# Performance work log

Hardware: AMD Instinct MI355X
Metric: run time of the kernel (lower is better)

Reference implementation:

```python
import jax, jax.numpy as jnp
import numpy as np

EPS = 1e-4

def safe_clamp(x, max_val):
    # nan -> 0, +inf -> max_val, -inf -> -max_val, then clamp to [-max_val, max_val]
    x = jnp.where(jnp.isnan(x), 0.0, x)
    x = jnp.where(jnp.isinf(x) & (x > 0), max_val, x)
    x = jnp.where(jnp.isinf(x) & (x < 0), -max_val, x)
    return jnp.clip(x, -max_val, max_val)

def setup_inputs() -> dict:
    key = jax.random.key(0)
    k1, k2 = jax.random.split(key)
    hidden_states = jax.random.normal(k1, (4, 4096, 2048), dtype=jnp.float32)
    ln_weight = jnp.ones((2048,), dtype=jnp.float32)
    ln_bias = jnp.zeros((2048,), dtype=jnp.float32)
    gate_weight = jax.random.normal(k2, (64, 2048), dtype=jnp.float32) * 0.01
    return {"hidden_states": hidden_states, "ln_weight": ln_weight,
            "ln_bias": ln_bias, "gate_weight": gate_weight}

def reference(hidden_states, ln_weight, ln_bias, gate_weight):
    B, S, H = hidden_states.shape
    top_k = 2
    x = hidden_states.reshape(-1, H)  # (N, H)
    # LayerNorm(eps=1e-5)
    mu = jnp.mean(x, axis=-1, keepdims=True)
    var = jnp.mean((x - mu) ** 2, axis=-1, keepdims=True)
    x = (x - mu) * jax.lax.rsqrt(var + 1e-5) * ln_weight + ln_bias
    x = safe_clamp(x, 50.0)
    # gate: (N, H) @ (H, E)
    router_logits = jnp.clip(x @ gate_weight.T, -10.0, 10.0)
    # eval mode: no noise
    router_probs = jnp.clip(jax.nn.softmax(router_logits, axis=-1), EPS, 1.0)
    top_k_probs, top_k_indices = jax.lax.top_k(router_probs, top_k)
    prob_sum = jnp.maximum(jnp.sum(top_k_probs, axis=-1, keepdims=True), EPS)
    top_k_probs = top_k_probs / prob_sum
    return top_k_probs, top_k_indices, router_logits
```

## Files before the change

### kernel.cpp

```cpp
#include <hip/hip_runtime.h>
#include <math.h>

#define H 2048
#define E 64
#define MR 16
#define KCH 128
#define NCH 16
#define LR 136

typedef _Float16 half8  __attribute__((ext_vector_type(8)));
typedef _Float16 half4h __attribute__((ext_vector_type(4)));
typedef float    f32x4  __attribute__((ext_vector_type(4)));

#define MFMA16(A,B,C) __builtin_amdgcn_mfma_f32_16x16x32_f16(A,B,C,0,0,0)


__global__ __launch_bounds__(256) void prep_pack(const float* __restrict__ W,
        const float* __restrict__ lnw, _Float16* __restrict__ Bh,
        _Float16* __restrict__ Bl) {
    int idx  = blockIdx.x * 256 + threadIdx.x;
    int lane = idx & 63;
    int ks   = idx >> 8;
    int e  = ((idx >> 6) & 3) * 16 + (lane & 15);
    int k0 = ks * 32 + ((lane >> 4) << 3);
    half8 hh, ll;
    #pragma unroll
    for (int j = 0; j < 8; ++j) {
        float wf = lnw[k0 + j] * W[e * H + k0 + j];
        _Float16 h = (_Float16)wf;
        _Float16 l = (_Float16)((wf - (float)h) * 2048.0f);
        hh[j] = h; ll[j] = l;
    }
    *(half8*)&Bh[(long)idx * 8] = hh;
    *(half8*)&Bl[(long)idx * 8] = ll;
}

__global__ __launch_bounds__(256) void prep_sums(const float* __restrict__ W,
        const float* __restrict__ lnw, const float* __restrict__ lnb,
        float* __restrict__ csum, float* __restrict__ bsum) {
    __shared__ float rc[256], rb[256];
    int e = blockIdx.x, t = threadIdx.x;
    float cs = 0.f, bs = 0.f;
    #pragma unroll
    for (int j = 0; j < 8; ++j) {
        int k = t + j * 256;
        float w = W[e * H + k];
        cs += lnw[k] * w;
        bs += lnb[k] * w;
    }
    rc[t] = cs; rb[t] = bs;
    __syncthreads();
    for (int s = 128; s > 0; s >>= 1) {
        if (t < s) { rc[t] += rc[t + s]; rb[t] += rb[t + s]; }
        __syncthreads();
    }
    if (t == 0) { csum[e] = rc[0]; bsum[e] = rb[0]; }
}

__global__ __launch_bounds__(256, 6) void router_kernel(
    const float* __restrict__ X, const _Float16* __restrict__ Bh,
    const _Float16* __restrict__ Bl, const float* __restrict__ csum,
    const float* __restrict__ bsum, float* __restrict__ out, int nRows)
{
    __shared__ __align__(16) _Float16 Xh[2][MR][LR];
    __shared__ __align__(16) _Float16 Xl[2][MR][LR];
    __shared__ float C2[MR][E + 4];
    __shared__ float mu_s[MR], rs_s[MR];

    const int t    = threadIdx.x;
    const int lane = t & 63;
    const int et   = t >> 6;
    const int q    = lane >> 4;
    const int ln16 = lane & 15;
    const int rowR = t >> 4;
    const int cS   = t & 15;
    const long rowBase = (long)blockIdx.x * MR;
    const long iOff = (long)nRows * 2;
    const long lOff = (long)nRows * 4;

    const float4* X4 = (const float4*)X;
    const float4* Xrow = X4 + (rowBase + rowR) * 512;

    float sacc = 0.f, qacc = 0.f;

    auto convert = [&](const float4* vb, int buf) {
        #pragma unroll
        for (int j = 0; j < 2; ++j) {
            float4 v = vb[j];
            sacc += v.x + v.y + v.z + v.w;
            qacc += v.x * v.x + v.y * v.y + v.z * v.z + v.w * v.w;
            _Float16 h0 = (_Float16)v.x, h1 = (_Float16)v.y,
                     h2 = (_Float16)v.z, h3 = (_Float16)v.w;
            _Float16 l0 = (_Float16)((v.x - (float)h0) * 2048.f);
            _Float16 l1 = (_Float16)((v.y - (float)h1) * 2048.f);
            _Float16 l2 = (_Float16)((v.z - (float)h2) * 2048.f);
            _Float16 l3 = (_Float16)((v.w - (float)h3) * 2048.f);
            half4h hh = {h0, h1, h2, h3};
            half4h ll = {l0, l1, l2, l3};
            int col = (cS + j * 16) * 4;
            *(half4h*)&Xh[buf][rowR][col] = hh;
            *(half4h*)&Xl[buf][rowR][col] = ll;
        }
    };

    {
        float4 vb[2];
        #pragma unroll
        for (int j = 0; j < 2; ++j) vb[j] = Xrow[cS + j * 16];
        convert(vb, 0);
    }
    __syncthreads();

    f32x4 acc0 = (f32x4)0.f;
    f32x4 acc1 = (f32x4)0.f;

    for (int c = 0; c < NCH; ++c) {
        const int buf = c & 1;

        half8 Wh[4], Wl[4];
        #pragma unroll
        for (int ks = 0; ks < 4; ++ks) {
            int bo = (((c * 4 + ks) * 4 + et) * 64 + lane) * 8;
            Wh[ks] = *(const half8*)&Bh[bo];
            Wl[ks] = *(const half8*)&Bl[bo];
        }
        float4 vb[2];
        if (c + 1 < NCH) {
            #pragma unroll
            for (int j = 0; j < 2; ++j)
                vb[j] = Xrow[(c + 1) * 32 + cS + j * 16];
        }

        #pragma unroll
        for (int ks = 0; ks < 4; ++ks) {
            half8 Ah = *(const half8*)&Xh[buf][ln16][ks * 32 + q * 8];
            half8 Al = *(const half8*)&Xl[buf][ln16][ks * 32 + q * 8];
            acc0 = MFMA16(Ah, Wh[ks], acc0);
            acc1 = MFMA16(Ah, Wl[ks], acc1);
            acc1 = MFMA16(Al, Wh[ks], acc1);
        }

        if (c + 1 < NCH) convert(vb, buf ^ 1);
        __syncthreads();
    }

    {
        float s = sacc, qq = qacc;
        #pragma unroll
        for (int d = 1; d < 16; d <<= 1) {
            s  += __shfl_xor(s, d);
            qq += __shfl_xor(qq, d);
        }
        if (cS == 0) {
            float mu  = s * (1.f / H);
            float var = qq * (1.f / H) - mu * mu;
            mu_s[rowR] = mu;
            rs_s[rowR] = rsqrtf(var + 1e-5f);
        }
    }
    __syncthreads();

    {
        int n = et * 16 + ln16;
        float cs = csum[n], bs = bsum[n];
        #pragma unroll
        for (int reg = 0; reg < 4; ++reg) {
            int r = q * 4 + reg;
            float raw = acc0[reg] + acc1[reg] * (1.f / 2048.f);
            float lg = rs_s[r] * (raw - mu_s[r] * cs) + bs;
            lg = fminf(fmaxf(lg, -10.f), 10.f);
            out[lOff + (rowBase + r) * 64 + n] = lg;
            C2[r][n] = lg;
        }
    }
    __syncthreads();

    #pragma unroll
    for (int rr = 0; rr < 4; ++rr) {
        int r = et * 4 + rr;
        float l = C2[r][lane];
        float m = l;
        #pragma unroll
        for (int d = 1; d < 64; d <<= 1) m = fmaxf(m, __shfl_xor(m, d));
        float p = __expf(l - m);
        float ssum = p;
        #pragma unroll
        for (int d = 1; d < 64; d <<= 1) ssum += __shfl_xor(ssum, d);
        float prob = fminf(fmaxf(p / ssum, 1e-4f), 1.0f);

        float v1 = prob; int i1 = lane;
        #pragma unroll
        for (int d = 1; d < 64; d <<= 1) {
            float ov = __shfl_xor(v1, d);
            int   oi = __shfl_xor(i1, d);
            if (ov > v1 || (ov == v1 && oi < i1)) { v1 = ov; i1 = oi; }
        }
        float v2 = (lane == i1) ? -1.f : prob; int i2 = lane;
        #pragma unroll
        for (int d = 1; d < 64; d <<= 1) {
            float ov = __shfl_xor(v2, d);
            int   oi = __shfl_xor(i2, d);
            if (ov > v2 || (ov == v2 && oi < i2)) { v2 = ov; i2 = oi; }
        }
        if (lane == 0) {
            float ps = fmaxf(v1 + v2, 1e-4f);
            long rg_ = rowBase + r;
            out[rg_ * 2 + 0] = v1 / ps;
            out[rg_ * 2 + 1] = v2 / ps;
            out[iOff + rg_ * 2 + 0] = (float)i1;
            out[iOff + rg_ * 2 + 1] = (float)i2;
        }
    }
}

extern "C" void kernel_launch(void* const* d_in, const int* in_sizes, int n_in,
                              void* d_out, int out_size, void* d_ws, size_t ws_size,
                              hipStream_t stream) {
    const float* X   = (const float*)d_in[0];
    const float* lnw = (const float*)d_in[1];
    const float* lnb = (const float*)d_in[2];
    const float* W   = (const float*)d_in[3];
    float* outp = (float*)d_out;

    _Float16* Bh = (_Float16*)d_ws;
    _Float16* Bl = Bh + H * E;
    float* csum  = (float*)(Bl + H * E);
    float* bsum  = csum + E;

    int N = in_sizes[0] / H;

    prep_pack<<<(H * E / 8) / 256, 256, 0, stream>>>(W, lnw, Bh, Bl);
    prep_sums<<<E, 256, 0, stream>>>(W, lnw, lnb, csum, bsum);
    router_kernel<<<N / MR, 256, 0, stream>>>(X, Bh, Bl, csum, bsum, outp, N);
}
```

Before: 214.8 us.

## Deepen X/W prefetch pipeline, fuse prep kernels, relax occupancy bound

Merges the two weight-preparation kernels into one 64-block launch, removing a kernel launch. The main router loop is unrolled by two with ping-pong register sets for W fragments and X prefetch, so X is loaded two chunks ahead and W one chunk ahead, hiding global load latency behind the MFMAs. Launch bounds drop from 6 to 4 waves per SIMD to make room for the extra registers, which trades occupancy for more in-flight loads per wave.

```diff
diff --git a/kernel.cpp b/kernel.cpp
--- a/kernel.cpp
+++ b/kernel.cpp
@@ -4,7 +4,6 @@
 #define H 2048
 #define E 64
 #define MR 16
-#define KCH 128
 #define NCH 16
 #define LR 136
 
@@ -15,49 +14,48 @@
 #define MFMA16(A,B,C) __builtin_amdgcn_mfma_f32_16x16x32_f16(A,B,C,0,0,0)
 
 
-__global__ __launch_bounds__(256) void prep_pack(const float* __restrict__ W,
-        const float* __restrict__ lnw, _Float16* __restrict__ Bh,
-        _Float16* __restrict__ Bl) {
-    int idx  = blockIdx.x * 256 + threadIdx.x;
-    int lane = idx & 63;
-    int ks   = idx >> 8;
-    int e  = ((idx >> 6) & 3) * 16 + (lane & 15);
-    int k0 = ks * 32 + ((lane >> 4) << 3);
-    half8 hh, ll;
-    #pragma unroll
-    for (int j = 0; j < 8; ++j) {
-        float wf = lnw[k0 + j] * W[e * H + k0 + j];
-        _Float16 h = (_Float16)wf;
-        _Float16 l = (_Float16)((wf - (float)h) * 2048.0f);
-        hh[j] = h; ll[j] = l;
-    }
-    *(half8*)&Bh[(long)idx * 8] = hh;
-    *(half8*)&Bl[(long)idx * 8] = ll;
+__global__ __launch_bounds__(256) void prep_fused(const float* __restrict__ W,
+        const float* __restrict__ lnw, const float* __restrict__ lnb,
+        _Float16* __restrict__ Bh, _Float16* __restrict__ Bl,
+        float* __restrict__ csum, float* __restrict__ bsum) {
+    {
+        int idx  = blockIdx.x * 256 + threadIdx.x;
+        int lane = idx & 63;
+        int e  = ((idx >> 6) & 3) * 16 + (lane & 15);
+        int k0 = (idx >> 8) * 32 + ((lane >> 4) << 3);
+        half8 hh, ll;
+        #pragma unroll
+        for (int j = 0; j < 8; ++j) {
+            float wf = lnw[k0 + j] * W[e * H + k0 + j];
+            _Float16 h = (_Float16)wf;
+            _Float16 l = (_Float16)((wf - (float)h) * 2048.0f);
+            hh[j] = h; ll[j] = l;
+        }
+        *(half8*)&Bh[(long)idx * 8] = hh;
+        *(half8*)&Bl[(long)idx * 8] = ll;
+    }
+    {
+        __shared__ float rc[256], rb[256];
+        int e = blockIdx.x, t = threadIdx.x;
+        float cs = 0.f, bs = 0.f;
+        #pragma unroll
+        for (int j = 0; j < 8; ++j) {
+            int k = t + j * 256;
+            float w = W[e * H + k];
+            cs += lnw[k] * w;
+            bs += lnb[k] * w;
+        }
+        rc[t] = cs; rb[t] = bs;
+        __syncthreads();
+        for (int s = 128; s > 0; s >>= 1) {
+            if (t < s) { rc[t] += rc[t + s]; rb[t] += rb[t + s]; }
+            __syncthreads();
+        }
+        if (t == 0) { csum[e] = rc[0]; bsum[e] = rb[0]; }
+    }
 }
 
-__global__ __launch_bounds__(256) void prep_sums(const float* __restrict__ W,
-        const float* __restrict__ lnw, const float* __restrict__ lnb,
-        float* __restrict__ csum, float* __restrict__ bsum) {
-    __shared__ float rc[256], rb[256];
-    int e = blockIdx.x, t = threadIdx.x;
-    float cs = 0.f, bs = 0.f;
-    #pragma unroll
-    for (int j = 0; j < 8; ++j) {
-        int k = t + j * 256;
-        float w = W[e * H + k];
-        cs += lnw[k] * w;
-        bs += lnb[k] * w;
-    }
-    rc[t] = cs; rb[t] = bs;
-    __syncthreads();
-    for (int s = 128; s > 0; s >>= 1) {
-        if (t < s) { rc[t] += rc[t + s]; rb[t] += rb[t + s]; }
-        __syncthreads();
-    }
-    if (t == 0) { csum[e] = rc[0]; bsum[e] = rb[0]; }
-}
-
-__global__ __launch_bounds__(256, 6) void router_kernel(
+__global__ __launch_bounds__(256, 4) void router_kernel(
     const float* __restrict__ X, const _Float16* __restrict__ Bh,
     const _Float16* __restrict__ Bl, const float* __restrict__ csum,
     const float* __restrict__ bsum, float* __restrict__ out, int nRows)
@@ -78,10 +76,12 @@
     const long iOff = (long)nRows * 2;
     const long lOff = (long)nRows * 4;
 
-    const float4* X4 = (const float4*)X;
-    const float4* Xrow = X4 + (rowBase + rowR) * 512;
+    const float4* Xrow = (const float4*)X + (rowBase + rowR) * 512;
 
     float sacc = 0.f, qacc = 0.f;
+
+    f32x4 acc0 = (f32x4)0.f;
+    f32x4 acc1 = (f32x4)0.f;
 
     auto convert = [&](const float4* vb, int buf) {
         #pragma unroll
@@ -102,35 +102,20 @@
             *(half4h*)&Xl[buf][rowR][col] = ll;
         }
     };
-
-    {
-        float4 vb[2];
-        #pragma unroll
-        for (int j = 0; j < 2; ++j) vb[j] = Xrow[cS + j * 16];
-        convert(vb, 0);
-    }
-    __syncthreads();
-
-    f32x4 acc0 = (f32x4)0.f;
-    f32x4 acc1 = (f32x4)0.f;
-
-    for (int c = 0; c < NCH; ++c) {
-        const int buf = c & 1;
-
-        half8 Wh[4], Wl[4];
+    auto loadW = [&](half8* Wh, half8* Wl, int c) {
         #pragma unroll
         for (int ks = 0; ks < 4; ++ks) {
             int bo = (((c * 4 + ks) * 4 + et) * 64 + lane) * 8;
             Wh[ks] = *(const half8*)&Bh[bo];
             Wl[ks] = *(const half8*)&Bl[bo];
         }
-        float4 vb[2];
-        if (c + 1 < NCH) {
-            #pragma unroll
-            for (int j = 0; j < 2; ++j)
-                vb[j] = Xrow[(c + 1) * 32 + cS + j * 16];
-        }
-
+    };
+    auto loadX = [&](float4* vb, int c) {
+        #pragma unroll
+        for (int j = 0; j < 2; ++j)
+            vb[j] = Xrow[c * 32 + cS + j * 16];
+    };
+    auto mfmaC = [&](const half8* Wh, const half8* Wl, int buf) {
         #pragma unroll
         for (int ks = 0; ks < 4; ++ks) {
             half8 Ah = *(const half8*)&Xh[buf][ln16][ks * 32 + q * 8];
@@ -139,8 +124,31 @@
             acc1 = MFMA16(Ah, Wl[ks], acc1);
             acc1 = MFMA16(Al, Wh[ks], acc1);
         }
-
-        if (c + 1 < NCH) convert(vb, buf ^ 1);
+    };
+
+    half8 WAh[4], WAl[4], WBh[4], WBl[4];
+    float4 vbA[2], vbB[2];
+
+    {
+        float4 v0[2];
+        loadX(v0, 0);
+        loadW(WAh, WAl, 0);
+        loadX(vbA, 1);
+        convert(v0, 0);
+    }
+    __syncthreads();
+
+    for (int c = 0; c < NCH; c += 2) {
+        loadW(WBh, WBl, c + 1);
+        if (c + 2 < NCH) loadX(vbB, c + 2);
+        mfmaC(WAh, WAl, 0);
+        convert(vbA, 1);
+        __syncthreads();
+
+        if (c + 2 < NCH) loadW(WAh, WAl, c + 2);
+        if (c + 3 < NCH) loadX(vbA, c + 3);
+        mfmaC(WBh, WBl, 1);
+        if (c + 2 < NCH) convert(vbB, 0);
         __syncthreads();
     }
 
@@ -229,7 +237,6 @@
 
     int N = in_sizes[0] / H;
 
-    prep_pack<<<(H * E / 8) / 256, 256, 0, stream>>>(W, lnw, Bh, Bl);
-    prep_sums<<<E, 256, 0, stream>>>(W, lnw, lnb, csum, bsum);
+    prep_fused<<<64, 256, 0, stream>>>(W, lnw, lnb, Bh, Bl, csum, bsum);
     router_kernel<<<N / MR, 256, 0, stream>>>(X, Bh, Bl, csum, bsum, outp, N);
 }
```

Result: slower. 247.2 us (+15.1%).
